# Performance work log

Hardware: AMD Instinct MI355X
Metric: run time of the kernel (lower is better)

## Reference

```python
import jax, jax.numpy as jnp
import numpy as np

NUM_NET = 2
V = 100000
D = 128
B = 4096
K = 5
NS = 10
HYP1 = 0.1
HYP2 = 0.1
HYP3 = 0.1


def setup_inputs() -> dict:
    key = jax.random.key(0)
    ks = jax.random.split(key, 10)
    ri = lambda k, shape: jax.random.randint(k, shape, 0, V, dtype=jnp.int32)
    return {
        "node_tables": jax.random.normal(ks[0], (NUM_NET, V, D), jnp.float32) * 0.1,
        "neigh_tables": jax.random.normal(ks[1], (NUM_NET, V, D), jnp.float32) * 0.1,
        "nodes_idx": ri(ks[2], (NUM_NET, B)),
        "neigh_idx": ri(ks[3], (NUM_NET, B, K)),
        "role_idx": ri(ks[4], (NUM_NET, NUM_NET, B)),
        "neg_main": ri(ks[5], (NUM_NET, B, K * NS)),
        "neg_node": ri(ks[6], (NUM_NET, NUM_NET, B, 1 * NS)),
        "neg_cross": ri(ks[7], (NUM_NET, NUM_NET, B, K * NS)),
        "neg_role": ri(ks[8], (NUM_NET, NUM_NET, B, 1 * NS)),
    }


def _pos_loss(ctx, node):
    # ctx: (B, M, D), node: (B, D) -> mean over all logsigmoid(ctx . node)
    return jax.nn.log_sigmoid(jnp.einsum("bmd,bd->bm", ctx, node)).mean()


def _neg_loss(neg_ctx, node):
    # ctx embeddings are negated: logsigmoid(-(neg . node)), sum over samples, mean over batch
    return jax.nn.log_sigmoid(-jnp.einsum("bmd,bd->bm", neg_ctx, node)).sum(axis=1).mean()


def reference(node_tables, neigh_tables, nodes_idx, neigh_idx, role_idx,
              neg_main, neg_node, neg_cross, neg_role):
    cost = []
    for i in range(NUM_NET):
        node_emb = node_tables[i][nodes_idx[i]]          # (B, D)
        # main SGNS loss on view i (neigh tables)
        neigh_emb = neigh_tables[i][neigh_idx[i]]        # (B, K, D)
        c = _pos_loss(neigh_emb, node_emb) + _neg_loss(neigh_tables[i][neg_main[i]], node_emb)
        cost.append(c)
        # cross-view node alignment (node tables of j at same node indices)
        for j in range(NUM_NET):
            if j != i:
                ctx = node_tables[j][nodes_idx[i]][:, None, :]   # (B, 1, D)
                c = _pos_loss(ctx, node_emb) + _neg_loss(node_tables[j][neg_node[i, j]], node_emb)
                cost.append(HYP1 * c)
        # cross-view neighbor loss (neigh tables of j at view-i neighbor indices)
        for j in range(NUM_NET):
            if j != i:
                ctx = neigh_tables[j][neigh_idx[i]]              # (B, K, D)
                c = _pos_loss(ctx, node_emb) + _neg_loss(neigh_tables[j][neg_cross[i, j]], node_emb)
                cost.append(HYP2 * c)
        # role-based loss (node tables of all j at role indices)
        for j in range(NUM_NET):
            ctx = node_tables[j][role_idx[i, j]][:, None, :]     # (B, 1, D)
            c = _pos_loss(ctx, node_emb) + _neg_loss(node_tables[j][neg_role[i, j]], node_emb)
            cost.append(HYP3 * c)
    total = cost[0]
    for c in cost[1:]:
        total = total + c
    return -total / len(cost)
```

## Files before the change

kernel.cpp:

```cpp
#include <hip/hip_runtime.h>
#include <utility>

#define NUM_NET 2
#define V 100000
#define D 128
#define B 4096
#define K 5
#define NS 10

#define W_A (1.0f/20480.0f)
#define W_B (1.0f/4096.0f)
#define W_C (0.1f/4096.0f)
#define W_D (0.1f/20480.0f)

#define NBINS 64
#define DEPTH 4

template <class F, int... Is>
__device__ __forceinline__ void sfor_impl(F&& f, std::integer_sequence<int, Is...>) {
    (f(std::integral_constant<int, Is>{}), ...);
}
template <int N, class F>
__device__ __forceinline__ void sfor(F&& f) {
    sfor_impl((F&&)f, std::make_integer_sequence<int, N>{});
}

template <int CTRL>
__device__ __forceinline__ float dpp_xadd(float v) {
    int r = __builtin_amdgcn_update_dpp(0, __float_as_int(v), CTRL, 0xF, 0xF, true);
    return v + __int_as_float(r);
}

__device__ __forceinline__ float lsig(float x) {
    return fminf(x, 0.0f) - __logf(1.0f + __expf(-fabsf(x)));
}

__device__ __forceinline__ void gload2(float4& d0, float4& d1, const float* addr) {
    asm volatile("global_load_dwordx4 %0, %2, off\n\t"
                 "global_load_dwordx4 %1, %2, off offset:256"
                 : "=&v"(d0), "=&v"(d1)
                 : "v"(addr)
                 : "memory");
}

template <int N>
__device__ __forceinline__ void waitfor() {
    asm volatile("s_waitcnt vmcnt(%0)" :: "i"(N) : "memory");
    __builtin_amdgcn_sched_barrier(0);
}

__global__ __launch_bounds__(256) void rmne_main(
    const float* __restrict__ node_tables,
    const float* __restrict__ neigh_tables,
    const int*   __restrict__ nodes_idx,
    const int*   __restrict__ neigh_idx,
    const int*   __restrict__ role_idx,
    const int*   __restrict__ neg_main,
    const int*   __restrict__ neg_node,
    const int*   __restrict__ neg_cross,
    const int*   __restrict__ neg_role,
    float*       __restrict__ ws)
{
    const int tid  = threadIdx.x;
    const int lane = tid & 63;
    const int wave = tid >> 6;
    const int unit = blockIdx.x * 4 + wave;
    const int i = unit >> 12;
    const int b = unit & (B - 1);
    const int j = 1 - i;

    int pk[3];
    #pragma unroll
    for (int s = 0; s < 3; ++s) {
        int d = lane + 64 * s;
        int idx = 0; int tab = 0;
        if      (d <   5) { idx = neigh_idx[(i*B + b)*K + d];             tab = 2 + i; }
        else if (d <  55) { idx = neg_main[(i*B + b)*50 + (d-5)];         tab = 2 + i; }
        else if (d <  56) { idx = nodes_idx[i*B + b];                     tab = j;     }
        else if (d <  66) { idx = neg_node[((i*2+j)*B + b)*NS + (d-56)];  tab = j;     }
        else if (d <  71) { idx = neigh_idx[(i*B + b)*K + (d-66)];        tab = 2 + j; }
        else if (d < 121) { idx = neg_cross[((i*2+j)*B + b)*50 + (d-71)]; tab = 2 + j; }
        else if (d < 122) { idx = role_idx[(i*2+0)*B + b];                tab = 0;     }
        else if (d < 132) { idx = neg_role[((i*2+0)*B + b)*NS + (d-122)]; tab = 0;     }
        else if (d < 133) { idx = role_idx[(i*2+1)*B + b];                tab = 1;     }
        else if (d < 143) { idx = neg_role[((i*2+1)*B + b)*NS + (d-133)]; tab = 1;     }
        pk[s] = idx | (tab << 20);
    }

    const int l16     = lane & 15;
    const int quarter = lane >> 4;
    const int nrow    = nodes_idx[i*B + b];
    const float* nep  = node_tables + ((size_t)i*V + (size_t)nrow)*D + l16*4;

    float4 c0b[DEPTH], c1b[DEPTH];
    float4 ne0, ne1;

    auto issue = [&](auto tc) {
        constexpr int T = decltype(tc)::value;
        constexpr int S = T >> 4;
        int src = (4*T + quarter) & 63;
        int p   = __shfl(pk[S], src, 64);
        int idx = p & 0xFFFFF;
        int tab = p >> 20;
        const float* base = (tab & 2) ? neigh_tables : node_tables;
        const float* addr = base + ((size_t)(tab & 1)*V + (size_t)idx)*D + l16*4;
        gload2(c0b[T & (DEPTH-1)], c1b[T & (DEPTH-1)], addr);
    };

    asm volatile("s_waitcnt vmcnt(0)" ::: "memory");

    gload2(ne0, ne1, nep);
    sfor<DEPTH>([&](auto tc) { issue(tc); });

    float accA = 0.0f, accB = 0.0f, accC = 0.0f, accG = 0.0f;

    sfor<36>([&](auto tc) {
        constexpr int T   = decltype(tc)::value;
        constexpr int INF = (36 - T) < DEPTH ? (36 - T) : DEPTH;
        waitfor<2*(INF-1)>();

        float4 c0 = c0b[T & (DEPTH-1)];
        float4 c1 = c1b[T & (DEPTH-1)];
        float pp = ne0.x*c0.x + ne0.y*c0.y + ne0.z*c0.z + ne0.w*c0.w
                 + ne1.x*c1.x + ne1.y*c1.y + ne1.z*c1.z + ne1.w*c1.w;
        pp = dpp_xadd<0xB1>(pp);
        pp = dpp_xadd<0x4E>(pp);
        pp = dpp_xadd<0x124>(pp);
        pp = dpp_xadd<0x128>(pp);

        if constexpr (T == 0) {
            accA += lsig(pp);
        } else if constexpr (T == 1) {
            float x  = (quarter == 0) ? pp : -pp;
            float mw = (quarter == 0) ? W_A : W_B;
            accG = fmaf(mw, lsig(x), accG);
        } else if constexpr (T <= 12) {
            accB += lsig(-pp);
        } else if constexpr (T == 13) {
            float x  = (quarter == 3) ? pp : -pp;
            float mw = (quarter == 3) ? W_C : W_B;
            accG = fmaf(mw, lsig(x), accG);
        } else if constexpr (T <= 15) {
            accC += lsig(-pp);
        } else if constexpr (T == 16) {
            float x  = (quarter >= 2) ? pp : -pp;
            float mw = (quarter >= 2) ? W_D : W_C;
            accG = fmaf(mw, lsig(x), accG);
        } else if constexpr (T == 17) {
            float x  = (quarter == 3) ? -pp : pp;
            float mw = (quarter == 3) ? W_C : W_D;
            accG = fmaf(mw, lsig(x), accG);
        } else if constexpr (T <= 29) {
            accC += lsig(-pp);
        } else if constexpr (T == 30) {
            float x = (quarter == 1) ? pp : -pp;
            accC += lsig(x);
        } else if constexpr (T <= 32) {
            accC += lsig(-pp);
        } else if constexpr (T == 33) {
            float x = (quarter == 0) ? pp : -pp;
            accC += lsig(x);
        } else if constexpr (T == 34) {
            accC += lsig(-pp);
        } else {
            float ls = lsig(-pp);
            accC += (quarter == 3) ? 0.0f : ls;
        }

        if constexpr (T + DEPTH < 36) issue(std::integral_constant<int, T + DEPTH>{});
    });

    float acc = W_A*accA + W_B*accB + W_C*accC + accG;

    acc += __shfl_xor(acc, 16, 64);
    acc += __shfl_xor(acc, 32, 64);

    __shared__ float wsum[4];
    if (lane == 0) wsum[wave] = acc;
    __syncthreads();
    if (tid == 0) {
        float s = wsum[0] + wsum[1] + wsum[2] + wsum[3];
        atomicAdd(ws + (blockIdx.x & (NBINS - 1)), s);
    }
}

__global__ void rmne_finalize(const float* __restrict__ ws, float* __restrict__ out)
{
    float v = ws[threadIdx.x];
    v += __shfl_xor(v, 1, 64);
    v += __shfl_xor(v, 2, 64);
    v += __shfl_xor(v, 4, 64);
    v += __shfl_xor(v, 8, 64);
    v += __shfl_xor(v, 16, 64);
    v += __shfl_xor(v, 32, 64);
    if (threadIdx.x == 0) out[0] = v * (-1.0f / 10.0f);
}

extern "C" void kernel_launch(void* const* d_in, const int* in_sizes, int n_in,
                              void* d_out, int out_size, void* d_ws, size_t ws_size,
                              hipStream_t stream) {
    const float* node_tables  = (const float*)d_in[0];
    const float* neigh_tables = (const float*)d_in[1];
    const int*   nodes_idx    = (const int*)d_in[2];
    const int*   neigh_idx    = (const int*)d_in[3];
    const int*   role_idx     = (const int*)d_in[4];
    const int*   neg_main     = (const int*)d_in[5];
    const int*   neg_node     = (const int*)d_in[6];
    const int*   neg_cross    = (const int*)d_in[7];
    const int*   neg_role     = (const int*)d_in[8];
    float* ws  = (float*)d_ws;
    float* out = (float*)d_out;

    hipMemsetAsync(ws, 0, NBINS * sizeof(float), stream);
    rmne_main<<<2048, 256, 0, stream>>>(node_tables, neigh_tables, nodes_idx, neigh_idx,
                                        role_idx, neg_main, neg_node, neg_cross, neg_role, ws);
    rmne_finalize<<<1, 64, 0, stream>>>(ws, out);
}
```

Before: 263.2 us.

## Bucket-sort gather entries by table row range for locality in embedding lookups

Adds a path that histograms every (context row, node row) pair by table and 128-row block, prefix-scans the counts, and scatters packed 64-bit entries into buckets. A processing kernel then handles one bucket per block, so each block's context-row gathers fall in a narrow address range and should hit cache better than fully random access. In exchange it adds four extra launches, two passes of global atomics, and about 9 MB of entry writes and reads, and the node row is now re-gathered for every entry. The old fused kernel is kept as a fallback when the workspace is too small.

```diff
diff --git a/kernel.cpp b/kernel.cpp
--- a/kernel.cpp
+++ b/kernel.cpp
@@ -14,7 +14,16 @@
 #define W_D (0.1f/20480.0f)
 
 #define NBINS 64
-#define DEPTH 4
+#define NENT  (8192*143)
+#define NBUCK 4096
+#define OFF_HIST   1024
+#define OFF_OFF    20480
+#define OFF_CUR    40960
+#define OFF_ENT    65536
+#define WS_NEEDED  (65536ULL + (unsigned long long)NENT*8ULL)
+
+typedef unsigned int u32;
+typedef unsigned long long u64;
 
 template <class F, int... Is>
 __device__ __forceinline__ void sfor_impl(F&& f, std::integer_sequence<int, Is...>) {
@@ -33,6 +42,140 @@
 
 __device__ __forceinline__ float lsig(float x) {
     return fminf(x, 0.0f) - __logf(1.0f + __expf(-fabsf(x)));
+}
+
+__device__ __forceinline__ void enum_entry(
+    u32 g, const int* nodes_idx, const int* neigh_idx, const int* role_idx,
+    const int* neg_main, const int* neg_node, const int* neg_cross,
+    const int* neg_role, int& idx, int& tab, int& cls, int& unit)
+{
+    unit = g / 143u;
+    int d = g - unit*143u;
+    int i = unit >> 12, b = unit & (B-1), j = 1 - i;
+    if      (d <   5) { idx = neigh_idx[(i*B+b)*K + d];             tab = 2+i; cls = 0; }
+    else if (d <  55) { idx = neg_main[(i*B+b)*50 + (d-5)];         tab = 2+i; cls = 1; }
+    else if (d <  56) { idx = nodes_idx[i*B+b];                     tab = j;   cls = 2; }
+    else if (d <  66) { idx = neg_node[((i*2+j)*B+b)*NS + (d-56)];  tab = j;   cls = 3; }
+    else if (d <  71) { idx = neigh_idx[(i*B+b)*K + (d-66)];        tab = 2+j; cls = 4; }
+    else if (d < 121) { idx = neg_cross[((i*2+j)*B+b)*50 + (d-71)]; tab = 2+j; cls = 3; }
+    else if (d < 122) { idx = role_idx[(i*2+0)*B+b];                tab = 0;   cls = 2; }
+    else if (d < 132) { idx = neg_role[((i*2+0)*B+b)*NS + (d-122)]; tab = 0;   cls = 3; }
+    else if (d < 133) { idx = role_idx[(i*2+1)*B+b];                tab = 1;   cls = 2; }
+    else              { idx = neg_role[((i*2+1)*B+b)*NS + (d-133)]; tab = 1;   cls = 3; }
+}
+
+__global__ __launch_bounds__(256) void rmne_hist(
+    const int* __restrict__ nodes_idx, const int* __restrict__ neigh_idx,
+    const int* __restrict__ role_idx,  const int* __restrict__ neg_main,
+    const int* __restrict__ neg_node,  const int* __restrict__ neg_cross,
+    const int* __restrict__ neg_role,  u32* __restrict__ hist)
+{
+    u32 g = blockIdx.x*256 + threadIdx.x;
+    if (g >= NENT) return;
+    int idx, tab, cls, unit;
+    enum_entry(g, nodes_idx, neigh_idx, role_idx, neg_main, neg_node,
+               neg_cross, neg_role, idx, tab, cls, unit);
+    atomicAdd(&hist[(tab<<10) | (idx>>7)], 1u);
+}
+
+__global__ __launch_bounds__(1024) void rmne_scan(
+    const u32* __restrict__ hist, u32* __restrict__ off, u32* __restrict__ cur)
+{
+    const u32 t = threadIdx.x, lane = t & 63, w = t >> 6;
+    u32 v0 = hist[4*t], v1 = hist[4*t+1], v2 = hist[4*t+2], v3 = hist[4*t+3];
+    u32 s = v0+v1+v2+v3;
+    u32 v = s;
+    #pragma unroll
+    for (int dlt = 1; dlt <= 32; dlt <<= 1) {
+        u32 u = __shfl_up(v, dlt, 64);
+        if (lane >= (u32)dlt) v += u;
+    }
+    __shared__ u32 p[16];
+    if (lane == 63) p[w] = v;
+    __syncthreads();
+    if (w == 0) {
+        u32 pv = (lane < 16) ? p[lane] : 0;
+        u32 pi = pv;
+        #pragma unroll
+        for (int dlt = 1; dlt <= 8; dlt <<= 1) {
+            u32 u = __shfl_up(pi, dlt, 64);
+            if (lane >= (u32)dlt) pi += u;
+        }
+        if (lane < 16) p[lane] = pi - pv;
+    }
+    __syncthreads();
+    u32 base = p[w] + v - s;
+    off[4*t]   = base;          cur[4*t]   = base;
+    off[4*t+1] = base+v0;       cur[4*t+1] = base+v0;
+    off[4*t+2] = base+v0+v1;    cur[4*t+2] = base+v0+v1;
+    off[4*t+3] = base+v0+v1+v2; cur[4*t+3] = base+v0+v1+v2;
+    if (t == 1023) off[4096] = base + s;
+}
+
+__global__ __launch_bounds__(256) void rmne_scatter(
+    const int* __restrict__ nodes_idx, const int* __restrict__ neigh_idx,
+    const int* __restrict__ role_idx,  const int* __restrict__ neg_main,
+    const int* __restrict__ neg_node,  const int* __restrict__ neg_cross,
+    const int* __restrict__ neg_role,  u32* __restrict__ cur,
+    u64* __restrict__ entries)
+{
+    u32 g = blockIdx.x*256 + threadIdx.x;
+    if (g >= NENT) return;
+    int idx, tab, cls, unit;
+    enum_entry(g, nodes_idx, neigh_idx, role_idx, neg_main, neg_node,
+               neg_cross, neg_role, idx, tab, cls, unit);
+    int i = unit >> 12, b = unit & (B-1);
+    int nrow = nodes_idx[i*B+b];
+    u64 ent = (u64)(u32)idx | ((u64)(u32)tab << 17)
+            | ((u64)(u32)((i<<17) | nrow) << 19) | ((u64)(u32)cls << 37);
+    u32 pos = atomicAdd(&cur[(tab<<10) | (idx>>7)], 1u);
+    entries[pos] = ent;
+}
+
+__global__ __launch_bounds__(256) void rmne_proc(
+    const float* __restrict__ node_tables, const float* __restrict__ neigh_tables,
+    const u32* __restrict__ off, const u64* __restrict__ entries,
+    float* __restrict__ ws)
+{
+    const u32 bucket = blockIdx.x;
+    const u32 start = off[bucket], end = off[bucket+1];
+    const int tid = threadIdx.x;
+    const int lane = tid & 63;
+    const int l16  = tid & 15;
+    const int q    = tid >> 4;
+
+    float acc = 0.0f;
+    for (u32 e = start + q; e < end; e += 16) {
+        u64 ent = entries[e];
+        int idx = (int)(ent & 0x1FFFF);
+        int tab = (int)((ent >> 17) & 3);
+        int ng  = (int)((ent >> 19) & 0x3FFFF);
+        int cls = (int)((ent >> 37) & 7);
+        const float* cbase = (tab & 2) ? neigh_tables : node_tables;
+        const float4* crow = (const float4*)(cbase + ((size_t)(tab&1)*V + (size_t)idx)*D) + l16*2;
+        const float4* nrow = (const float4*)(node_tables + ((size_t)(ng>>17)*V + (size_t)(ng&0x1FFFF))*D) + l16*2;
+        float4 c0 = crow[0], c1 = crow[1];
+        float4 n0 = nrow[0], n1 = nrow[1];
+        float pp = n0.x*c0.x + n0.y*c0.y + n0.z*c0.z + n0.w*c0.w
+                 + n1.x*c1.x + n1.y*c1.y + n1.z*c1.z + n1.w*c1.w;
+        pp = dpp_xadd<0xB1>(pp);
+        pp = dpp_xadd<0x4E>(pp);
+        pp = dpp_xadd<0x124>(pp);
+        pp = dpp_xadd<0x128>(pp);
+        float x   = (cls & 1) ? -pp : pp;
+        float mag = (cls == 0) ? W_A : (cls == 1) ? W_B : (cls == 4) ? W_D : W_C;
+        acc = fmaf(mag, lsig(x), acc);
+    }
+
+    acc += __shfl_xor(acc, 16, 64);
+    acc += __shfl_xor(acc, 32, 64);
+    __shared__ float wsum[4];
+    if (lane == 0) wsum[tid >> 6] = acc;
+    __syncthreads();
+    if (tid == 0) {
+        float s = wsum[0] + wsum[1] + wsum[2] + wsum[3];
+        atomicAdd(ws + (blockIdx.x & (NBINS-1)), s);
+    }
 }
 
 __device__ __forceinline__ void gload2(float4& d0, float4& d1, const float* addr) {
@@ -42,13 +185,12 @@
                  : "v"(addr)
                  : "memory");
 }
-
 template <int N>
 __device__ __forceinline__ void waitfor() {
     asm volatile("s_waitcnt vmcnt(%0)" :: "i"(N) : "memory");
     __builtin_amdgcn_sched_barrier(0);
 }
-
+#define DEPTH 4
 __global__ __launch_bounds__(256) void rmne_main(
     const float* __restrict__ node_tables,
     const float* __restrict__ neigh_tables,
@@ -68,7 +210,6 @@
     const int i = unit >> 12;
     const int b = unit & (B - 1);
     const int j = 1 - i;
-
     int pk[3];
     #pragma unroll
     for (int s = 0; s < 3; ++s) {
@@ -86,15 +227,12 @@
         else if (d < 143) { idx = neg_role[((i*2+1)*B + b)*NS + (d-133)]; tab = 1;     }
         pk[s] = idx | (tab << 20);
     }
-
     const int l16     = lane & 15;
     const int quarter = lane >> 4;
     const int nrow    = nodes_idx[i*B + b];
     const float* nep  = node_tables + ((size_t)i*V + (size_t)nrow)*D + l16*4;
-
     float4 c0b[DEPTH], c1b[DEPTH];
     float4 ne0, ne1;
-
     auto issue = [&](auto tc) {
         constexpr int T = decltype(tc)::value;
         constexpr int S = T >> 4;
@@ -106,19 +244,14 @@
         const float* addr = base + ((size_t)(tab & 1)*V + (size_t)idx)*D + l16*4;
         gload2(c0b[T & (DEPTH-1)], c1b[T & (DEPTH-1)], addr);
     };
-
     asm volatile("s_waitcnt vmcnt(0)" ::: "memory");
-
     gload2(ne0, ne1, nep);
     sfor<DEPTH>([&](auto tc) { issue(tc); });
-
     float accA = 0.0f, accB = 0.0f, accC = 0.0f, accG = 0.0f;
-
     sfor<36>([&](auto tc) {
         constexpr int T   = decltype(tc)::value;
         constexpr int INF = (36 - T) < DEPTH ? (36 - T) : DEPTH;
         waitfor<2*(INF-1)>();
-
         float4 c0 = c0b[T & (DEPTH-1)];
         float4 c1 = c1b[T & (DEPTH-1)];
         float pp = ne0.x*c0.x + ne0.y*c0.y + ne0.z*c0.z + ne0.w*c0.w
@@ -127,22 +260,18 @@
         pp = dpp_xadd<0x4E>(pp);
         pp = dpp_xadd<0x124>(pp);
         pp = dpp_xadd<0x128>(pp);
-
-        if constexpr (T == 0) {
-            accA += lsig(pp);
-        } else if constexpr (T == 1) {
+        if constexpr (T == 0) { accA += lsig(pp); }
+        else if constexpr (T == 1) {
             float x  = (quarter == 0) ? pp : -pp;
             float mw = (quarter == 0) ? W_A : W_B;
             accG = fmaf(mw, lsig(x), accG);
-        } else if constexpr (T <= 12) {
-            accB += lsig(-pp);
-        } else if constexpr (T == 13) {
+        } else if constexpr (T <= 12) { accB += lsig(-pp); }
+        else if constexpr (T == 13) {
             float x  = (quarter == 3) ? pp : -pp;
             float mw = (quarter == 3) ? W_C : W_B;
             accG = fmaf(mw, lsig(x), accG);
-        } else if constexpr (T <= 15) {
-            accC += lsig(-pp);
-        } else if constexpr (T == 16) {
+        } else if constexpr (T <= 15) { accC += lsig(-pp); }
+        else if constexpr (T == 16) {
             float x  = (quarter >= 2) ? pp : -pp;
             float mw = (quarter >= 2) ? W_D : W_C;
             accG = fmaf(mw, lsig(x), accG);
@@ -150,31 +279,24 @@
             float x  = (quarter == 3) ? -pp : pp;
             float mw = (quarter == 3) ? W_C : W_D;
             accG = fmaf(mw, lsig(x), accG);
-        } else if constexpr (T <= 29) {
-            accC += lsig(-pp);
-        } else if constexpr (T == 30) {
+        } else if constexpr (T <= 29) { accC += lsig(-pp); }
+        else if constexpr (T == 30) {
             float x = (quarter == 1) ? pp : -pp;
             accC += lsig(x);
-        } else if constexpr (T <= 32) {
-            accC += lsig(-pp);
-        } else if constexpr (T == 33) {
+        } else if constexpr (T <= 32) { accC += lsig(-pp); }
+        else if constexpr (T == 33) {
             float x = (quarter == 0) ? pp : -pp;
             accC += lsig(x);
-        } else if constexpr (T == 34) {
-            accC += lsig(-pp);
-        } else {
+        } else if constexpr (T == 34) { accC += lsig(-pp); }
+        else {
             float ls = lsig(-pp);
             accC += (quarter == 3) ? 0.0f : ls;
         }
-
         if constexpr (T + DEPTH < 36) issue(std::integral_constant<int, T + DEPTH>{});
     });
-
     float acc = W_A*accA + W_B*accB + W_C*accC + accG;
-
     acc += __shfl_xor(acc, 16, 64);
     acc += __shfl_xor(acc, 32, 64);
-
     __shared__ float wsum[4];
     if (lane == 0) wsum[wave] = acc;
     __syncthreads();
@@ -208,11 +330,29 @@
     const int*   neg_node     = (const int*)d_in[6];
     const int*   neg_cross    = (const int*)d_in[7];
     const int*   neg_role     = (const int*)d_in[8];
-    float* ws  = (float*)d_ws;
     float* out = (float*)d_out;
 
-    hipMemsetAsync(ws, 0, NBINS * sizeof(float), stream);
-    rmne_main<<<2048, 256, 0, stream>>>(node_tables, neigh_tables, nodes_idx, neigh_idx,
-                                        role_idx, neg_main, neg_node, neg_cross, neg_role, ws);
-    rmne_finalize<<<1, 64, 0, stream>>>(ws, out);
-}
+    if (ws_size >= WS_NEEDED) {
+        char* wsb = (char*)d_ws;
+        float* bins   = (float*)wsb;
+        u32*   hist   = (u32*)(wsb + OFF_HIST);
+        u32*   off    = (u32*)(wsb + OFF_OFF);
+        u32*   cur    = (u32*)(wsb + OFF_CUR);
+        u64*   ents   = (u64*)(wsb + OFF_ENT);
+        hipMemsetAsync(d_ws, 0, OFF_ENT, stream);
+        const int EB = (NENT + 255) / 256;
+        rmne_hist<<<EB, 256, 0, stream>>>(nodes_idx, neigh_idx, role_idx, neg_main,
+                                          neg_node, neg_cross, neg_role, hist);
+        rmne_scan<<<1, 1024, 0, stream>>>(hist, off, cur);
+        rmne_scatter<<<EB, 256, 0, stream>>>(nodes_idx, neigh_idx, role_idx, neg_main,
+                                             neg_node, neg_cross, neg_role, cur, ents);
+        rmne_proc<<<NBUCK, 256, 0, stream>>>(node_tables, neigh_tables, off, ents, bins);
+        rmne_finalize<<<1, 64, 0, stream>>>(bins, out);
+    } else {
+        float* ws = (float*)d_ws;
+        hipMemsetAsync(ws, 0, NBINS * sizeof(float), stream);
+        rmne_main<<<2048, 256, 0, stream>>>(node_tables, neigh_tables, nodes_idx, neigh_idx,
+                                            role_idx, neg_main, neg_node, neg_cross, neg_role, ws);
+        rmne_finalize<<<1, 64, 0, stream>>>(ws, out);
+    }
+}
```

Result: slower. 565.0 us (+114.6%).
